# Optimization experiments

Measured on AMD Instinct MI355X. Metric: run time of the kernel, lower is better.

Reference implementation:

```python
import jax, jax.numpy as jnp
import numpy as np

B, N, D = 2, 2048, 1024
H = 16                      # num_heads, head_dim = 64
E, K, CF = 4, 2, 1.0        # num_experts, top_k, capacity_factor
MLP_H = int(D * 4.0)        # dense Mlp hidden (mlp_ratio=4.0)
MOE_H = int(D * 0.25)       # expert hidden (hard-coded dim*0.25 in source)


def setup_inputs() -> dict:
    key = jax.random.key(0)
    ks = jax.random.split(key, 12)
    r = lambda k, shp, s=0.02: jax.random.normal(k, shp, jnp.float32) * s
    return dict(
        x=jax.random.normal(ks[0], (B, N, D), jnp.float32),
        noise=jax.random.normal(ks[1], (B, N, E), jnp.float32),
        ln1_g=jnp.ones((D,), jnp.float32), ln1_b=jnp.zeros((D,), jnp.float32),
        ln2_g=jnp.ones((D,), jnp.float32), ln2_b=jnp.zeros((D,), jnp.float32),
        w_qkv=r(ks[2], (3 * D, D)),
        w_proj=r(ks[3], (D, D)), b_proj=jnp.zeros((D,), jnp.float32),
        w_route=r(ks[4], (D, E), 0.05), b_route=jnp.zeros((E,), jnp.float32),
        w_noise=r(ks[5], (D, E), 0.05), b_noise=jnp.zeros((E,), jnp.float32),
        we1=r(ks[6], (E, D, MOE_H)), be1=jnp.zeros((E, MOE_H), jnp.float32),
        we2=r(ks[7], (E, MOE_H, D)), be2=jnp.zeros((E, D), jnp.float32),
        w_mlp1=r(ks[8], (D, MLP_H)), b_mlp1=jnp.zeros((MLP_H,), jnp.float32),
        w_mlp2=r(ks[9], (MLP_H, D)), b_mlp2=jnp.zeros((D,), jnp.float32),
    )


def _ln(x, g, b, eps=1e-5):
    mu = x.mean(-1, keepdims=True)
    var = ((x - mu) ** 2).mean(-1, keepdims=True)
    return (x - mu) * jax.lax.rsqrt(var + eps) * g + b


def _gelu(x):
    return jax.nn.gelu(x, approximate=False)  # torch nn.GELU default (erf)


def reference(x, noise, ln1_g, ln1_b, ln2_g, ln2_b, w_qkv, w_proj, b_proj,
              w_route, b_route, w_noise, b_noise, we1, be1, we2, be2,
              w_mlp1, b_mlp1, w_mlp2, b_mlp2):
    Bs, Ns, Ds = x.shape
    hd = Ds // H
    # --- attention branch ---
    x1 = _ln(x, ln1_g, ln1_b)
    qkv = (x1 @ w_qkv.T).reshape(Bs, Ns, 3, H, hd).transpose(2, 0, 3, 1, 4)
    q, k, v = qkv[0] * (hd ** -0.5), qkv[1], qkv[2]
    attn = jax.nn.softmax(jnp.einsum('bhnd,bhmd->bhnm', q, k), axis=-1)
    ao = jnp.einsum('bhnm,bhmd->bhnd', attn, v).transpose(0, 2, 1, 3).reshape(Bs, Ns, Ds)
    x = x + (ao @ w_proj.T + b_proj)
    # --- shared norm for mlp + moe ---
    x2 = _ln(x, ln2_g, ln2_b)
    # --- noisy top-k router ---
    logits = x2 @ w_route + b_route                  # [B,N,E]
    noisy = logits + noise * jax.nn.softplus(x2 @ w_noise + b_noise)
    topv, topi = jax.lax.top_k(noisy, K)             # [B,N,K]
    probs = jax.nn.softmax(topv, axis=-1)            # softmax over sparse logits == softmax over top-k
    T = Bs * Ns
    flat_x = x2.reshape(T, Ds)
    fidx = topi.reshape(T, K)
    rows = jnp.arange(T)[:, None]
    gate = jnp.zeros((T, E), noisy.dtype).at[rows, fidx].set(probs.reshape(T, K))
    capacity = int(T * K / E * CF)
    # --- capacity-limited dispatch / expert MLP / combine ---
    def dispatch(eid, W1, b1, W2, b2):
        mask = jnp.any(fidx == eid, axis=-1)                     # [T]
        order = jnp.argsort(jnp.logical_not(mask))               # stable: selected tokens first, in token order
        sel = order[:capacity]                                   # [C]
        valid = mask[sel].astype(flat_x.dtype)
        h = _gelu(flat_x[sel] @ W1 + b1)
        out = h @ W2 + b2
        w = gate[sel, eid] * valid
        return sel, out * w[:, None]
    sel, outw = jax.vmap(dispatch)(jnp.arange(E), we1, be1, we2, be2)   # [E,C], [E,C,D]
    moe = jnp.zeros_like(flat_x).at[sel.reshape(-1)].add(outw.reshape(-1, Ds)).reshape(Bs, Ns, Ds)
    # --- dense mlp branch ---
    mlp = _gelu(x2 @ w_mlp1 + b_mlp1) @ w_mlp2 + b_mlp2
    return x + mlp + moe
```

## Files before the change

kernel.cpp:

```cpp
#include <hip/hip_runtime.h>
#include <hip/hip_bf16.h>
#include <math.h>

typedef __bf16 bf16;
typedef __bf16 bf16x4 __attribute__((ext_vector_type(4)));
typedef __bf16 bf16x8 __attribute__((ext_vector_type(8)));
typedef float  f32x4  __attribute__((ext_vector_type(4)));
typedef short  s16x4  __attribute__((ext_vector_type(4)));

#define T_TOK 4096
#define DIM   1024
#define NHEAD 16
#define SEQ   2048
#define NEXP  4
#define CAP   2048
#define MLPH  4096
#define MOEH  256

__device__ __forceinline__ float gelu_exact(float v) {
    return 0.5f * v * (1.f + erff(v * 0.70710678118654752f));
}

struct HL { bf16 h, l; };
__device__ __forceinline__ HL split2(float v) {
    HL r; r.h = (bf16)v; r.l = (bf16)(v - (float)r.h); return r;
}

__device__ __forceinline__ float fast_exp2(float x) {
#if __has_builtin(__builtin_amdgcn_exp2f)
    return __builtin_amdgcn_exp2f(x);
#else
    return exp2f(x);
#endif
}

__device__ __forceinline__ f32x4 mfma16(bf16x4 a, bf16x4 b, f32x4 c) {
    return __builtin_amdgcn_mfma_f32_16x16x16bf16_1k(
        __builtin_bit_cast(s16x4, a), __builtin_bit_cast(s16x4, b), c, 0, 0, 0);
}

__device__ __forceinline__ void gload16(const bf16* gptr, bf16* lptr) {
    __builtin_amdgcn_global_load_lds(
        (const __attribute__((address_space(1))) unsigned int*)gptr,
        (__attribute__((address_space(3))) unsigned int*)lptr,
        16, 0, 0);
}

__device__ __forceinline__ bf16x8 sw_frag(const bf16* arr, int row, int cc) {
    return *(const bf16x8*)&arr[row * 64 + ((cc ^ (row & 7)) * 8)];
}
__device__ __forceinline__ bf16x4 v_frag(const bf16* arr, int d, int q) {
    return *(const bf16x4*)&arr[d * 64 + ((q ^ (d & 15)) * 4)];
}

__global__ __launch_bounds__(256)
void ln_split_kernel(const float* __restrict__ x, const float* __restrict__ g,
                     const float* __restrict__ b, bf16* __restrict__ oh, bf16* __restrict__ ol) {
    int wave = threadIdx.x >> 6, lane = threadIdx.x & 63;
    long t = (long)blockIdx.x * 4 + wave;
    const float* xr = x + t * DIM;
    float v[16];
    #pragma unroll
    for (int i = 0; i < 16; i++) v[i] = xr[i * 64 + lane];
    float s = 0.f, s2 = 0.f;
    #pragma unroll
    for (int i = 0; i < 16; i++) { s += v[i]; s2 += v[i] * v[i]; }
    #pragma unroll
    for (int m = 1; m < 64; m <<= 1) { s += __shfl_xor(s, m); s2 += __shfl_xor(s2, m); }
    float mu  = s * (1.f / DIM);
    float var = s2 * (1.f / DIM) - mu * mu;
    float rs  = 1.f / sqrtf(var + 1e-5f);
    #pragma unroll
    for (int i = 0; i < 16; i++) {
        int d = i * 64 + lane;
        HL sp = split2((v[i] - mu) * rs * g[d] + b[d]);
        oh[t * DIM + d] = sp.h; ol[t * DIM + d] = sp.l;
    }
}

__global__ __launch_bounds__(256)
void split_pair_kernel(const float* __restrict__ in, bf16* __restrict__ h, bf16* __restrict__ l) {
    long i0 = ((long)blockIdx.x * 256 + threadIdx.x) * 4;
    f32x4 v = *(const f32x4*)&in[i0];
    bf16x4 vh, vl;
    #pragma unroll
    for (int j = 0; j < 4; j++) { HL sp = split2(v[j]); vh[j] = sp.h; vl[j] = sp.l; }
    *(bf16x4*)&h[i0] = vh; *(bf16x4*)&l[i0] = vl;
}

__global__ __launch_bounds__(256)
void transpose_conv_kernel(const float* __restrict__ in, bf16* __restrict__ out, int R, int C) {
    __shared__ bf16 tile[32][33];
    long bo = (long)blockIdx.z * R * C;
    in += bo; out += bo;
    int c0 = blockIdx.x * 32, r0 = blockIdx.y * 32;
    int tx = threadIdx.x & 31, ty = threadIdx.x >> 5;
    #pragma unroll
    for (int i = 0; i < 32; i += 8)
        tile[ty + i][tx] = (bf16)in[(long)(r0 + ty + i) * C + c0 + tx];
    __syncthreads();
    #pragma unroll
    for (int i = 0; i < 32; i += 8)
        out[(long)(c0 + ty + i) * R + r0 + tx] = tile[tx][ty + i];
}

__global__ __launch_bounds__(256)
void gemm_qkv(const bf16* __restrict__ Ah_g, const bf16* __restrict__ Al_g,
              const bf16* __restrict__ Bh_g, const bf16* __restrict__ Bl_g,
              bf16* __restrict__ Qh_g, bf16* __restrict__ Ql_g,
              bf16* __restrict__ Kh_g, bf16* __restrict__ Kl_g,
              bf16* __restrict__ VtH, bf16* __restrict__ VtL) {
    const int K = DIM;
    __shared__ alignas(16) bf16 Ah[8192], Al[8192], Bh[8192], Bl[8192];
    int tid = threadIdx.x;
    int wave = tid >> 6, lane = tid & 63;
    int l16 = lane & 15, l4 = lane >> 4;
    int wr = (wave >> 1) * 64, wc = (wave & 1) * 64;
    int row0 = blockIdx.y * 128, col0 = blockIdx.x * 128;
    int r8s = lane >> 3;
    int colb = ((lane & 7) ^ r8s) * 8;
    f32x4 acc[4][4] = {};
    for (int k0 = 0; k0 < K; k0 += 64) {
        #pragma unroll
        for (int p = 0; p < 4; p++) {
            int rl = p * 32 + wave * 8 + r8s;
            int lb = p * 2048 + wave * 512;
            gload16(&Ah_g[(long)(row0 + rl) * K + k0 + colb], &Ah[lb]);
            gload16(&Al_g[(long)(row0 + rl) * K + k0 + colb], &Al[lb]);
            gload16(&Bh_g[(long)(col0 + rl) * K + k0 + colb], &Bh[lb]);
            gload16(&Bl_g[(long)(col0 + rl) * K + k0 + colb], &Bl[lb]);
        }
        __syncthreads();
        #pragma unroll
        for (int ks = 0; ks < 2; ks++) {
            bf16x8 ah[4], al[4], bh[4], bl[4];
            #pragma unroll
            for (int i = 0; i < 4; i++) {
                ah[i] = sw_frag(Ah, wr + i*16 + l16, ks*4 + l4);
                al[i] = sw_frag(Al, wr + i*16 + l16, ks*4 + l4);
            }
            #pragma unroll
            for (int j = 0; j < 4; j++) {
                bh[j] = sw_frag(Bh, wc + j*16 + l16, ks*4 + l4);
                bl[j] = sw_frag(Bl, wc + j*16 + l16, ks*4 + l4);
            }
            #pragma unroll
            for (int i = 0; i < 4; i++)
                #pragma unroll
                for (int j = 0; j < 4; j++) {
                    acc[i][j] = __builtin_amdgcn_mfma_f32_16x16x32_bf16(ah[i], bh[j], acc[i][j], 0, 0, 0);
                    acc[i][j] = __builtin_amdgcn_mfma_f32_16x16x32_bf16(ah[i], bl[j], acc[i][j], 0, 0, 0);
                    acc[i][j] = __builtin_amdgcn_mfma_f32_16x16x32_bf16(al[i], bh[j], acc[i][j], 0, 0, 0);
                }
        }
        __syncthreads();
    }
    if (col0 < 2048) {
        bool isQ = (col0 < 1024);
        bf16* oh = isQ ? Qh_g : Kh_g;
        bf16* ol = isQ ? Ql_g : Kl_g;
        float qscale = isQ ? 0.18033688011112043f : 1.0f;
        #pragma unroll
        for (int i = 0; i < 4; i++)
            #pragma unroll
            for (int r = 0; r < 4; r++) {
                int t = row0 + wr + i * 16 + l4 * 4 + r;
                int bq = t >> 11, s = t & 2047;
                #pragma unroll
                for (int j = 0; j < 4; j++) {
                    int col = (col0 + wc + j * 16 + l16) & 1023;
                    int hh = col >> 6, dl = col & 63;
                    long o = ((long)(bq * NHEAD + hh) * SEQ + s) * 64 + dl;
                    HL sp = split2(acc[i][j][r] * qscale);
                    oh[o] = sp.h;
                    if (!isQ) ol[o] = sp.l;
                }
            }
    } else {
        #pragma unroll
        for (int i = 0; i < 4; i++) {
            int s0 = row0 + wr + i * 16 + l4 * 4;
            int b = s0 >> 11, sl = s0 & 2047;
            #pragma unroll
            for (int j = 0; j < 4; j++) {
                int d = col0 - 2048 + wc + j * 16 + l16;
                int h = d >> 6, dl = d & 63;
                long base = ((long)(b * NHEAD + h) * 64 + dl) * SEQ + (sl ^ ((dl & 1) << 2));
                bf16x4 vh, vl;
                #pragma unroll
                for (int r = 0; r < 4; r++) { HL sp = split2(acc[i][j][r]); vh[r] = sp.h; vl[r] = sp.l; }
                *(bf16x4*)&VtH[base] = vh;
                *(bf16x4*)&VtL[base] = vl;
            }
        }
    }
}

__global__ __launch_bounds__(512, 4)
void flash_attn(const bf16* __restrict__ Qh_g,
                const bf16* __restrict__ Kh_g, const bf16* __restrict__ Kl_g,
                const bf16* __restrict__ VtH_g, const bf16* __restrict__ VtL_g,
                bf16* __restrict__ aoh, bf16* __restrict__ aol) {
    __shared__ alignas(16) bf16 KhS[2][4096], KlS[2][4096], VhS[2][4096], VlS[2][4096];
    int tid = threadIdx.x;
    int wave = tid >> 6, lane = tid & 63;
    int l16 = lane & 15, l4 = lane >> 4;
    int bid = blockIdx.x;
    int bh = bid & 31;
    int b = bh >> 4, h = bh & 15;
    int q0 = (bid >> 5) * 128;

    bf16x8 qfh[2];
    {
        const bf16* qh = Qh_g + ((long)bh * SEQ + q0 + wave * 16 + l16) * 64;
        #pragma unroll
        for (int ks = 0; ks < 2; ks++)
            qfh[ks] = *(const bf16x8*)&qh[ks * 32 + l4 * 8];
    }
    int r8 = lane >> 3;
    int c8 = lane & 7;
    const bf16* kh_g = Kh_g + (long)bh * SEQ * 64;
    const bf16* kl_g = Kl_g + (long)bh * SEQ * 64;
    const bf16* vh_g = VtH_g + (long)bh * 64 * SEQ;
    const bf16* vl_g = VtL_g + (long)bh * 64 * SEQ;

    float m_s = -1e30f, l_s = 0.f;
    f32x4 accO[4] = {};

    auto stage = [&](int c0, int bsel) {
        int R0 = wave * 8;
        int row = R0 + r8;
        int ksw = (c8 ^ r8) * 8;
        int vsw = (c8 ^ ((wave * 4 + (r8 >> 1)) & 7)) * 8;
        gload16(&kh_g[(long)(c0 + row) * 64 + ksw], &KhS[bsel][R0 * 64]);
        gload16(&kl_g[(long)(c0 + row) * 64 + ksw], &KlS[bsel][R0 * 64]);
        gload16(&vh_g[(long)row * SEQ + c0 + vsw], &VhS[bsel][R0 * 64]);
        gload16(&vl_g[(long)row * SEQ + c0 + vsw], &VlS[bsel][R0 * 64]);
    };

    auto compute = [&](const bf16* KhT, const bf16* KlT, const bf16* VhT, const bf16* VlT) {
        f32x4 st[4] = {};
        __builtin_amdgcn_s_setprio(1);
        #pragma unroll
        for (int ks = 0; ks < 2; ks++) {
            #pragma unroll
            for (int i = 0; i < 4; i++) {
                bf16x8 akh = sw_frag(KhT, i * 16 + l16, ks * 4 + l4);
                bf16x8 akl = sw_frag(KlT, i * 16 + l16, ks * 4 + l4);
                st[i] = __builtin_amdgcn_mfma_f32_16x16x32_bf16(akh, qfh[ks], st[i], 0, 0, 0);
                st[i] = __builtin_amdgcn_mfma_f32_16x16x32_bf16(akl, qfh[ks], st[i], 0, 0, 0);
            }
        }
        __builtin_amdgcn_s_setprio(0);
        float mx = st[0][0];
        #pragma unroll
        for (int i = 0; i < 4; i++)
            #pragma unroll
            for (int r = 0; r < 4; r++) mx = fmaxf(mx, st[i][r]);
        mx = fmaxf(mx, __shfl_xor(mx, 16));
        mx = fmaxf(mx, __shfl_xor(mx, 32));
        if (!__all(mx <= m_s + 8.f)) {
            float mnew = fmaxf(m_s, mx);
            float alpha = fast_exp2(m_s - mnew);
            l_s *= alpha;
            #pragma unroll
            for (int i = 0; i < 4; i++)
                #pragma unroll
                for (int r = 0; r < 4; r++) accO[i][r] *= alpha;
            m_s = mnew;
        }
        float psum = 0.f;
        bf16x4 ph[4];
        #pragma unroll
        for (int kb = 0; kb < 4; kb++)
            #pragma unroll
            for (int r = 0; r < 4; r++) {
                float pv = fast_exp2(st[kb][r] - m_s);
                psum += pv;
                ph[kb][r] = (bf16)pv;
            }
        psum += __shfl_xor(psum, 16);
        psum += __shfl_xor(psum, 32);
        l_s += psum;
        __builtin_amdgcn_s_setprio(1);
        #pragma unroll
        for (int kb = 0; kb < 4; kb++) {
            #pragma unroll
            for (int i = 0; i < 4; i++) {
                bf16x4 avh = v_frag(VhT, i * 16 + l16, kb * 4 + l4);
                bf16x4 avl = v_frag(VlT, i * 16 + l16, kb * 4 + l4);
                accO[i] = mfma16(avh, ph[kb], accO[i]);
                accO[i] = mfma16(avl, ph[kb], accO[i]);
            }
        }
        __builtin_amdgcn_s_setprio(0);
    };

    const int NT = SEQ / 64;
    stage(0, 0);
    #pragma unroll 1
    for (int t = 0; t < NT; t += 2) {
        stage((t + 1) * 64, 1);
        asm volatile("s_waitcnt vmcnt(4)" ::: "memory");
        __builtin_amdgcn_sched_barrier(0);
        __builtin_amdgcn_s_barrier();
        compute(KhS[0], KlS[0], VhS[0], VlS[0]);
        asm volatile("" ::: "memory");
        __builtin_amdgcn_s_barrier();
        if (t + 2 < NT) {
            stage((t + 2) * 64, 0);
            asm volatile("s_waitcnt vmcnt(4)" ::: "memory");
        } else {
            asm volatile("s_waitcnt vmcnt(0)" ::: "memory");
        }
        __builtin_amdgcn_sched_barrier(0);
        __builtin_amdgcn_s_barrier();
        compute(KhS[1], KlS[1], VhS[1], VlS[1]);
        asm volatile("" ::: "memory");
        __builtin_amdgcn_s_barrier();
    }

    float inv = 1.f / l_s;
    int q = q0 + wave * 16 + l16;
    #pragma unroll
    for (int i = 0; i < 4; i++) {
        bf16x4 oh4, ol4;
        #pragma unroll
        for (int r = 0; r < 4; r++) { HL sp = split2(accO[i][r] * inv); oh4[r] = sp.h; ol4[r] = sp.l; }
        long o = ((long)(b * SEQ + q)) * DIM + h * 64 + i * 16 + l4 * 4;
        *(bf16x4*)&aoh[o] = oh4;
        *(bf16x4*)&aol[o] = ol4;
    }
}

__global__ __launch_bounds__(256)
void gemm_proj(const bf16* __restrict__ Ah_g, const bf16* __restrict__ Al_g,
               const bf16* __restrict__ Bh_g, const bf16* __restrict__ Bl_g,
               const float* __restrict__ bias, const float* __restrict__ res,
               float* __restrict__ C, int N, int K) {
    __shared__ alignas(16) bf16 Ah[8192], Al[8192], Bh[8192], Bl[8192];
    int tid = threadIdx.x;
    int wave = tid >> 6, lane = tid & 63;
    int l16 = lane & 15, l4 = lane >> 4;
    int wr = (wave >> 1) * 64, wc = (wave & 1) * 64;
    int row0 = blockIdx.y * 128, col0 = blockIdx.x * 128;
    int r8s = lane >> 3;
    int colb = ((lane & 7) ^ r8s) * 8;
    f32x4 acc[4][4] = {};
    for (int k0 = 0; k0 < K; k0 += 64) {
        #pragma unroll
        for (int p = 0; p < 4; p++) {
            int rl = p * 32 + wave * 8 + r8s;
            int lb = p * 2048 + wave * 512;
            gload16(&Ah_g[(long)(row0 + rl) * K + k0 + colb], &Ah[lb]);
            gload16(&Al_g[(long)(row0 + rl) * K + k0 + colb], &Al[lb]);
            gload16(&Bh_g[(long)(col0 + rl) * K + k0 + colb], &Bh[lb]);
            gload16(&Bl_g[(long)(col0 + rl) * K + k0 + colb], &Bl[lb]);
        }
        __syncthreads();
        #pragma unroll
        for (int ks = 0; ks < 2; ks++) {
            bf16x8 ah[4], al[4], bh[4], bl[4];
            #pragma unroll
            for (int i = 0; i < 4; i++) {
                ah[i] = sw_frag(Ah, wr + i*16 + l16, ks*4 + l4);
                al[i] = sw_frag(Al, wr + i*16 + l16, ks*4 + l4);
            }
            #pragma unroll
            for (int j = 0; j < 4; j++) {
                bh[j] = sw_frag(Bh, wc + j*16 + l16, ks*4 + l4);
                bl[j] = sw_frag(Bl, wc + j*16 + l16, ks*4 + l4);
            }
            #pragma unroll
            for (int i = 0; i < 4; i++)
                #pragma unroll
                for (int j = 0; j < 4; j++) {
                    acc[i][j] = __builtin_amdgcn_mfma_f32_16x16x32_bf16(ah[i], bh[j], acc[i][j], 0, 0, 0);
                    acc[i][j] = __builtin_amdgcn_mfma_f32_16x16x32_bf16(ah[i], bl[j], acc[i][j], 0, 0, 0);
                    acc[i][j] = __builtin_amdgcn_mfma_f32_16x16x32_bf16(al[i], bh[j], acc[i][j], 0, 0, 0);
                }
        }
        __syncthreads();
    }
    #pragma unroll
    for (int i = 0; i < 4; i++)
        #pragma unroll
        for (int r = 0; r < 4; r++) {
            int grow = row0 + wr + i * 16 + l4 * 4 + r;
            #pragma unroll
            for (int j = 0; j < 4; j++) {
                int gcol = col0 + wc + j * 16 + l16;
                long o = (long)grow * N + gcol;
                C[o] = acc[i][j][r] + bias[gcol] + res[o];
            }
        }
}

template<bool BIAS, bool GELU, bool GATHER, int OUT_MODE>
__global__ __launch_bounds__(256)
void gemm_bt(const bf16* __restrict__ A, const bf16* __restrict__ Bt,
             const float* __restrict__ bias,
             bf16* __restrict__ Cbf, float* __restrict__ Cf,
             const int* __restrict__ rowmap, const float* __restrict__ roww,
             int M, int N, int K,
             long eA, long eB, long ebias, long eMap, long eC) {
    int ez = blockIdx.z;
    A += (long)ez * eA; Bt += (long)ez * eB;
    if (BIAS) bias += (long)ez * ebias;
    if (GATHER || OUT_MODE == 3) rowmap += (long)ez * eMap;
    if (OUT_MODE == 3) roww += (long)ez * eMap;
    if (OUT_MODE == 0) Cbf += (long)ez * eC;

    __shared__ alignas(16) bf16 As[8192];
    __shared__ alignas(16) bf16 Bs[8192];
    int tid = threadIdx.x;
    int wave = tid >> 6, lane = tid & 63;
    int l16 = lane & 15, l4 = lane >> 4;
    int wr = (wave >> 1) * 64, wc = (wave & 1) * 64;
    int row0 = blockIdx.y * 128, col0 = blockIdx.x * 128;
    int r8s = lane >> 3;
    int colb = ((lane & 7) ^ r8s) * 8;

    long arow[4];
    #pragma unroll
    for (int p = 0; p < 4; p++) {
        long gr = row0 + p * 32 + wave * 8 + r8s;
        if (GATHER) gr = rowmap[gr];
        arow[p] = gr;
    }
    f32x4 acc[4][4] = {};
    for (int k0 = 0; k0 < K; k0 += 64) {
        #pragma unroll
        for (int p = 0; p < 4; p++) {
            int rl = p * 32 + wave * 8 + r8s;
            int lb = p * 2048 + wave * 512;
            gload16(&A[arow[p] * K + k0 + colb], &As[lb]);
            gload16(&Bt[(long)(col0 + rl) * K + k0 + colb], &Bs[lb]);
        }
        __syncthreads();
        #pragma unroll
        for (int ks = 0; ks < 2; ks++) {
            bf16x8 af[4], bfr[4];
            #pragma unroll
            for (int i = 0; i < 4; i++) af[i]  = sw_frag(As, wr + i*16 + l16, ks*4 + l4);
            #pragma unroll
            for (int j = 0; j < 4; j++) bfr[j] = sw_frag(Bs, wc + j*16 + l16, ks*4 + l4);
            #pragma unroll
            for (int i = 0; i < 4; i++)
                #pragma unroll
                for (int j = 0; j < 4; j++)
                    acc[i][j] = __builtin_amdgcn_mfma_f32_16x16x32_bf16(af[i], bfr[j], acc[i][j], 0, 0, 0);
        }
        __syncthreads();
    }
    #pragma unroll
    for (int i = 0; i < 4; i++)
        #pragma unroll
        for (int r = 0; r < 4; r++) {
            int grow = row0 + wr + i * 16 + l4 * 4 + r;
            int st = 0; float sw = 0.f;
            if (OUT_MODE == 3) { st = rowmap[grow]; sw = roww[grow]; }
            #pragma unroll
            for (int j = 0; j < 4; j++) {
                int gcol = col0 + wc + j * 16 + l16;
                float v = acc[i][j][r];
                if (BIAS) v += bias[gcol];
                if (GELU) v = gelu_exact(v);
                if (OUT_MODE == 0) {
                    Cbf[(long)grow * N + gcol] = (bf16)v;
                } else if (OUT_MODE == 2) {
                    long o = (long)grow * N + gcol;
                    Cf[o] += v;
                } else {
                    atomicAdd(&Cf[(long)st * N + gcol], sw * v);
                }
            }
        }
}

__global__ __launch_bounds__(256)
void routing_kernel(const float* __restrict__ xres, const float* __restrict__ g,
                    const float* __restrict__ b, const float* __restrict__ w_route,
                    const float* __restrict__ b_route, const float* __restrict__ w_noise,
                    const float* __restrict__ b_noise, const float* __restrict__ noise,
                    int* __restrict__ topi, float* __restrict__ topp,
                    bf16* __restrict__ x2b) {
    int wave = threadIdx.x >> 6, lane = threadIdx.x & 63;
    long t = (long)blockIdx.x * 4 + wave;
    const float* xr = xres + t * DIM;
    float v[16];
    #pragma unroll
    for (int i = 0; i < 16; i++) v[i] = xr[i * 64 + lane];
    float s = 0.f, s2 = 0.f;
    #pragma unroll
    for (int i = 0; i < 16; i++) { s += v[i]; s2 += v[i] * v[i]; }
    #pragma unroll
    for (int m = 1; m < 64; m <<= 1) { s += __shfl_xor(s, m); s2 += __shfl_xor(s2, m); }
    float mu  = s * (1.f / DIM);
    float var = s2 * (1.f / DIM) - mu * mu;
    float rs  = 1.f / sqrtf(var + 1e-5f);
    float accr[4] = {0.f,0.f,0.f,0.f}, accn[4] = {0.f,0.f,0.f,0.f};
    #pragma unroll
    for (int i = 0; i < 16; i++) {
        int d = i * 64 + lane;
        float n = (v[i] - mu) * rs * g[d] + b[d];
        x2b[t * DIM + d] = (bf16)n;
        #pragma unroll
        for (int e = 0; e < 4; e++) {
            accr[e] += n * w_route[d * 4 + e];
            accn[e] += n * w_noise[d * 4 + e];
        }
    }
    #pragma unroll
    for (int e = 0; e < 4; e++)
        #pragma unroll
        for (int m = 1; m < 64; m <<= 1) {
            accr[e] += __shfl_xor(accr[e], m);
            accn[e] += __shfl_xor(accn[e], m);
        }
    if (lane == 0) {
        float nz[4];
        #pragma unroll
        for (int e = 0; e < 4; e++) {
            float logit = accr[e] + b_route[e];
            float si = accn[e] + b_noise[e];
            float sp = si > 0.f ? si + log1pf(expf(-si)) : log1pf(expf(si));
            nz[e] = logit + noise[t * 4 + e] * sp;
        }
        int i1 = 0;
        #pragma unroll
        for (int e = 1; e < 4; e++) if (nz[e] > nz[i1]) i1 = e;
        int i2 = -1; float v2 = -1e30f;
        #pragma unroll
        for (int e = 0; e < 4; e++) if (e != i1 && nz[e] > v2) { v2 = nz[e]; i2 = e; }
        float ex = expf(v2 - nz[i1]);
        topi[t * 2]     = i1; topi[t * 2 + 1] = i2;
        topp[t * 2]     = 1.f / (1.f + ex);
        topp[t * 2 + 1] = ex / (1.f + ex);
    }
}

__global__ __launch_bounds__(256)
void dispatch_kernel(const int* __restrict__ topi, const float* __restrict__ topp,
                     int* __restrict__ sel, float* __restrict__ wgt) {
    int e = threadIdx.x >> 6, lane = threadIdx.x & 63;
    int cnt = 0;
    for (int c = 0; c < T_TOK; c += 64) {
        int t = c + lane;
        int i0 = topi[t * 2], i1 = topi[t * 2 + 1];
        bool m = (i0 == e) || (i1 == e);
        unsigned long long bal = __ballot(m);
        int pos = cnt + __popcll(bal & ((1ull << lane) - 1ull));
        if (m && pos < CAP) {
            sel[e * CAP + pos] = t;
            wgt[e * CAP + pos] = (i0 == e) ? topp[t * 2] : topp[t * 2 + 1];
        }
        cnt += (int)__popcll(bal);
    }
    if (cnt > CAP) cnt = CAP;
    for (int pos = cnt + lane; pos < CAP; pos += 64) {
        sel[e * CAP + pos] = 0;
        wgt[e * CAP + pos] = 0.f;
    }
}

extern "C" void kernel_launch(void* const* d_in, const int* in_sizes, int n_in,
                              void* d_out, int out_size, void* d_ws, size_t ws_size,
                              hipStream_t stream) {
    (void)in_sizes; (void)n_in; (void)out_size; (void)ws_size;
    const float* x       = (const float*)d_in[0];
    const float* noise   = (const float*)d_in[1];
    const float* ln1_g   = (const float*)d_in[2];
    const float* ln1_b   = (const float*)d_in[3];
    const float* ln2_g   = (const float*)d_in[4];
    const float* ln2_b   = (const float*)d_in[5];
    const float* w_qkv   = (const float*)d_in[6];
    const float* w_proj  = (const float*)d_in[7];
    const float* b_proj  = (const float*)d_in[8];
    const float* w_route = (const float*)d_in[9];
    const float* b_route = (const float*)d_in[10];
    const float* w_noise = (const float*)d_in[11];
    const float* b_noise = (const float*)d_in[12];
    const float* we1     = (const float*)d_in[13];
    const float* be1     = (const float*)d_in[14];
    const float* we2     = (const float*)d_in[15];
    const float* be2     = (const float*)d_in[16];
    const float* w_mlp1  = (const float*)d_in[17];
    const float* b_mlp1  = (const float*)d_in[18];
    const float* w_mlp2  = (const float*)d_in[19];
    const float* b_mlp2  = (const float*)d_in[20];
    float* d_outf = (float*)d_out;

    const size_t MB = 1024 * 1024;
    char* ws = (char*)d_ws;
    bf16* x1h = (bf16*)(ws);
    bf16* x1l = (bf16*)(ws + 8 * MB);
    bf16* aoh = (bf16*)(ws);
    bf16* aol = (bf16*)(ws + 8 * MB);
    bf16* w_mlp1T = (bf16*)(ws);
    bf16* w_mlp2T = (bf16*)(ws + 8 * MB);
    bf16* wqkvh = (bf16*)(ws + 16 * MB);
    bf16* wqkvl = (bf16*)(ws + 22 * MB);
    bf16* we1T  = (bf16*)(ws + 16 * MB);
    bf16* we2T  = (bf16*)(ws + 18 * MB);
    bf16* h_e   = (bf16*)(ws + 20 * MB);
    bf16* wprojh = (bf16*)(ws + 28 * MB);
    bf16* wprojl = (bf16*)(ws + 30 * MB);
    bf16* Qh = (bf16*)(ws + 32 * MB);
    bf16* Ql = (bf16*)(ws + 40 * MB);
    bf16* Kh = (bf16*)(ws + 48 * MB);
    bf16* Kl = (bf16*)(ws + 56 * MB);
    bf16* h_mlp = (bf16*)(ws + 32 * MB);
    bf16*  VtH  = (bf16*)(ws + 64 * MB);
    bf16*  VtL  = (bf16*)(ws + 72 * MB);
    bf16*  x2b  = (bf16*)(ws + 64 * MB);
    int*   topi = (int*)(ws + 72 * MB);
    float* topp = (float*)(ws + 72 * MB + 32768);
    int*   sel  = (int*)(ws + 72 * MB + 65536);
    float* wgt  = (float*)(ws + 72 * MB + 98304);

    ln_split_kernel<<<T_TOK/4, 256, 0, stream>>>(x, ln1_g, ln1_b, x1h, x1l);
    split_pair_kernel<<<(3*DIM*DIM)/1024, 256, 0, stream>>>(w_qkv, wqkvh, wqkvl);
    split_pair_kernel<<<(DIM*DIM)/1024,   256, 0, stream>>>(w_proj, wprojh, wprojl);

    gemm_qkv<<<dim3(3*DIM/128, T_TOK/128), 256, 0, stream>>>(
        x1h, x1l, wqkvh, wqkvl, Qh, Ql, Kh, Kl, VtH, VtL);

    flash_attn<<<dim3(32 * (SEQ/128)), 512, 0, stream>>>(Qh, Kh, Kl, VtH, VtL, aoh, aol);

    gemm_proj<<<dim3(DIM/128, T_TOK/128), 256, 0, stream>>>(
        aoh, aol, wprojh, wprojl, b_proj, x, d_outf, DIM, DIM);

    routing_kernel<<<T_TOK/4, 256, 0, stream>>>(d_outf, ln2_g, ln2_b, w_route, b_route,
                                                w_noise, b_noise, noise, topi, topp, x2b);
    dispatch_kernel<<<1, 256, 0, stream>>>(topi, topp, sel, wgt);

    transpose_conv_kernel<<<dim3(MLPH/32, DIM/32, 1),    256, 0, stream>>>(w_mlp1, w_mlp1T, DIM, MLPH);
    transpose_conv_kernel<<<dim3(DIM/32, MLPH/32, 1),    256, 0, stream>>>(w_mlp2, w_mlp2T, MLPH, DIM);
    transpose_conv_kernel<<<dim3(MOEH/32, DIM/32, NEXP), 256, 0, stream>>>(we1, we1T, DIM, MOEH);
    transpose_conv_kernel<<<dim3(DIM/32, MOEH/32, NEXP), 256, 0, stream>>>(we2, we2T, MOEH, DIM);

    gemm_bt<true,true,false,0><<<dim3(MLPH/128, T_TOK/128), 256, 0, stream>>>(
        x2b, w_mlp1T, b_mlp1, h_mlp, nullptr, nullptr, nullptr, T_TOK, MLPH, DIM,
        0, 0, 0, 0, 0);
    gemm_bt<true,false,false,2><<<dim3(DIM/128, T_TOK/128), 256, 0, stream>>>(
        h_mlp, w_mlp2T, b_mlp2, nullptr, d_outf, nullptr, nullptr, T_TOK, DIM, MLPH,
        0, 0, 0, 0, 0);

    gemm_bt<true,true,true,0><<<dim3(MOEH/128, CAP/128, NEXP), 256, 0, stream>>>(
        x2b, we1T, be1, h_e, nullptr, sel, nullptr, CAP, MOEH, DIM,
        0, (long)MOEH*DIM, MOEH, CAP, (long)CAP*MOEH);
    gemm_bt<true,false,false,3><<<dim3(DIM/128, CAP/128, NEXP), 256, 0, stream>>>(
        h_e, we2T, be2, nullptr, d_outf, sel, wgt, CAP, DIM, MOEH,
        (long)CAP*MOEH, (long)DIM*MOEH, DIM, CAP, 0);
}
```

Measured before the change: 635.2 us.

## Interleave V hi/lo splits and use 16x16x32 MFMA in PV product

The hi and lo bf16 halves of V are now stored interleaved in one transposed buffer. The attention kernel duplicates each P value to match that pairing, so a single 16x16x32 bf16 MFMA computes P·(Vh+Vl) where two 16x16x16 MFMAs were used before. This halves the PV MFMA issue count and fuses the two LDS fragment reads into one wider read. The cost is a new LDS swizzle and staging pattern, plus a V buffer of the same total size with a new layout.

```diff
diff --git a/kernel.cpp b/kernel.cpp
--- a/kernel.cpp
+++ b/kernel.cpp
@@ -6,7 +6,6 @@
 typedef __bf16 bf16x4 __attribute__((ext_vector_type(4)));
 typedef __bf16 bf16x8 __attribute__((ext_vector_type(8)));
 typedef float  f32x4  __attribute__((ext_vector_type(4)));
-typedef short  s16x4  __attribute__((ext_vector_type(4)));
 
 #define T_TOK 4096
 #define DIM   1024
@@ -34,11 +33,6 @@
 #endif
 }
 
-__device__ __forceinline__ f32x4 mfma16(bf16x4 a, bf16x4 b, f32x4 c) {
-    return __builtin_amdgcn_mfma_f32_16x16x16bf16_1k(
-        __builtin_bit_cast(s16x4, a), __builtin_bit_cast(s16x4, b), c, 0, 0, 0);
-}
-
 __device__ __forceinline__ void gload16(const bf16* gptr, bf16* lptr) {
     __builtin_amdgcn_global_load_lds(
         (const __attribute__((address_space(1))) unsigned int*)gptr,
@@ -48,9 +42,6 @@
 
 __device__ __forceinline__ bf16x8 sw_frag(const bf16* arr, int row, int cc) {
     return *(const bf16x8*)&arr[row * 64 + ((cc ^ (row & 7)) * 8)];
-}
-__device__ __forceinline__ bf16x4 v_frag(const bf16* arr, int d, int q) {
-    return *(const bf16x4*)&arr[d * 64 + ((q ^ (d & 15)) * 4)];
 }
 
 __global__ __launch_bounds__(256)
@@ -109,7 +100,7 @@
               const bf16* __restrict__ Bh_g, const bf16* __restrict__ Bl_g,
               bf16* __restrict__ Qh_g, bf16* __restrict__ Ql_g,
               bf16* __restrict__ Kh_g, bf16* __restrict__ Kl_g,
-              bf16* __restrict__ VtH, bf16* __restrict__ VtL) {
+              bf16* __restrict__ VtI) {
     const int K = DIM;
     __shared__ alignas(16) bf16 Ah[8192], Al[8192], Bh[8192], Bl[8192];
     int tid = threadIdx.x;
@@ -185,12 +176,14 @@
             for (int j = 0; j < 4; j++) {
                 int d = col0 - 2048 + wc + j * 16 + l16;
                 int h = d >> 6, dl = d & 63;
-                long base = ((long)(b * NHEAD + h) * 64 + dl) * SEQ + (sl ^ ((dl & 1) << 2));
-                bf16x4 vh, vl;
+                long base = ((long)(b * NHEAD + h) * 64 + dl) * (2 * SEQ) + 2 * sl;
+                bf16x8 vi;
                 #pragma unroll
-                for (int r = 0; r < 4; r++) { HL sp = split2(acc[i][j][r]); vh[r] = sp.h; vl[r] = sp.l; }
-                *(bf16x4*)&VtH[base] = vh;
-                *(bf16x4*)&VtL[base] = vl;
+                for (int r = 0; r < 4; r++) {
+                    HL sp = split2(acc[i][j][r]);
+                    vi[2 * r] = sp.h; vi[2 * r + 1] = sp.l;
+                }
+                *(bf16x8*)&VtI[base] = vi;
             }
         }
     }
@@ -199,9 +192,9 @@
 __global__ __launch_bounds__(512, 4)
 void flash_attn(const bf16* __restrict__ Qh_g,
                 const bf16* __restrict__ Kh_g, const bf16* __restrict__ Kl_g,
-                const bf16* __restrict__ VtH_g, const bf16* __restrict__ VtL_g,
+                const bf16* __restrict__ VtI_g,
                 bf16* __restrict__ aoh, bf16* __restrict__ aol) {
-    __shared__ alignas(16) bf16 KhS[2][4096], KlS[2][4096], VhS[2][4096], VlS[2][4096];
+    __shared__ alignas(16) bf16 KhS[2][4096], KlS[2][4096], VIS[2][8192];
     int tid = threadIdx.x;
     int wave = tid >> 6, lane = tid & 63;
     int l16 = lane & 15, l4 = lane >> 4;
@@ -219,10 +212,10 @@
     }
     int r8 = lane >> 3;
     int c8 = lane & 7;
+    int r4 = lane >> 4, c16 = lane & 15;
     const bf16* kh_g = Kh_g + (long)bh * SEQ * 64;
     const bf16* kl_g = Kl_g + (long)bh * SEQ * 64;
-    const bf16* vh_g = VtH_g + (long)bh * 64 * SEQ;
-    const bf16* vl_g = VtL_g + (long)bh * 64 * SEQ;
+    const bf16* vI_g = VtI_g + (long)bh * 64 * (2 * SEQ);
 
     float m_s = -1e30f, l_s = 0.f;
     f32x4 accO[4] = {};
@@ -231,14 +224,17 @@
         int R0 = wave * 8;
         int row = R0 + r8;
         int ksw = (c8 ^ r8) * 8;
-        int vsw = (c8 ^ ((wave * 4 + (r8 >> 1)) & 7)) * 8;
         gload16(&kh_g[(long)(c0 + row) * 64 + ksw], &KhS[bsel][R0 * 64]);
         gload16(&kl_g[(long)(c0 + row) * 64 + ksw], &KlS[bsel][R0 * 64]);
-        gload16(&vh_g[(long)row * SEQ + c0 + vsw], &VhS[bsel][R0 * 64]);
-        gload16(&vl_g[(long)row * SEQ + c0 + vsw], &VlS[bsel][R0 * 64]);
+        #pragma unroll
+        for (int q = 0; q < 2; q++) {
+            int d0 = R0 + q * 4 + r4;
+            gload16(&vI_g[(long)d0 * (2 * SEQ) + 2 * c0 + ((c16 ^ (d0 & 15)) * 8)],
+                    &VIS[bsel][(R0 + q * 4) * 128]);
+        }
     };
 
-    auto compute = [&](const bf16* KhT, const bf16* KlT, const bf16* VhT, const bf16* VlT) {
+    auto compute = [&](const bf16* KhT, const bf16* KlT, const bf16* VIT) {
         f32x4 st[4] = {};
         __builtin_amdgcn_s_setprio(1);
         #pragma unroll
@@ -270,14 +266,15 @@
             m_s = mnew;
         }
         float psum = 0.f;
-        bf16x4 ph[4];
+        bf16x8 pw[4];
         #pragma unroll
         for (int kb = 0; kb < 4; kb++)
             #pragma unroll
             for (int r = 0; r < 4; r++) {
                 float pv = fast_exp2(st[kb][r] - m_s);
                 psum += pv;
-                ph[kb][r] = (bf16)pv;
+                bf16 pb = (bf16)pv;
+                pw[kb][2 * r] = pb; pw[kb][2 * r + 1] = pb;
             }
         psum += __shfl_xor(psum, 16);
         psum += __shfl_xor(psum, 32);
@@ -287,10 +284,9 @@
         for (int kb = 0; kb < 4; kb++) {
             #pragma unroll
             for (int i = 0; i < 4; i++) {
-                bf16x4 avh = v_frag(VhT, i * 16 + l16, kb * 4 + l4);
-                bf16x4 avl = v_frag(VlT, i * 16 + l16, kb * 4 + l4);
-                accO[i] = mfma16(avh, ph[kb], accO[i]);
-                accO[i] = mfma16(avl, ph[kb], accO[i]);
+                int d = i * 16 + l16;
+                bf16x8 av = *(const bf16x8*)&VIT[d * 128 + (((kb * 4 + l4) ^ (d & 15)) * 8)];
+                accO[i] = __builtin_amdgcn_mfma_f32_16x16x32_bf16(av, pw[kb], accO[i], 0, 0, 0);
             }
         }
         __builtin_amdgcn_s_setprio(0);
@@ -304,7 +300,7 @@
         asm volatile("s_waitcnt vmcnt(4)" ::: "memory");
         __builtin_amdgcn_sched_barrier(0);
         __builtin_amdgcn_s_barrier();
-        compute(KhS[0], KlS[0], VhS[0], VlS[0]);
+        compute(KhS[0], KlS[0], VIS[0]);
         asm volatile("" ::: "memory");
         __builtin_amdgcn_s_barrier();
         if (t + 2 < NT) {
@@ -315,7 +311,7 @@
         }
         __builtin_amdgcn_sched_barrier(0);
         __builtin_amdgcn_s_barrier();
-        compute(KhS[1], KlS[1], VhS[1], VlS[1]);
+        compute(KhS[1], KlS[1], VIS[1]);
         asm volatile("" ::: "memory");
         __builtin_amdgcn_s_barrier();
     }
@@ -611,8 +607,7 @@
     bf16* Kh = (bf16*)(ws + 48 * MB);
     bf16* Kl = (bf16*)(ws + 56 * MB);
     bf16* h_mlp = (bf16*)(ws + 32 * MB);
-    bf16*  VtH  = (bf16*)(ws + 64 * MB);
-    bf16*  VtL  = (bf16*)(ws + 72 * MB);
+    bf16*  VtI  = (bf16*)(ws + 64 * MB);
     bf16*  x2b  = (bf16*)(ws + 64 * MB);
     int*   topi = (int*)(ws + 72 * MB);
     float* topp = (float*)(ws + 72 * MB + 32768);
@@ -624,9 +619,9 @@
     split_pair_kernel<<<(DIM*DIM)/1024,   256, 0, stream>>>(w_proj, wprojh, wprojl);
 
     gemm_qkv<<<dim3(3*DIM/128, T_TOK/128), 256, 0, stream>>>(
-        x1h, x1l, wqkvh, wqkvl, Qh, Ql, Kh, Kl, VtH, VtL);
-
-    flash_attn<<<dim3(32 * (SEQ/128)), 512, 0, stream>>>(Qh, Kh, Kl, VtH, VtL, aoh, aol);
+        x1h, x1l, wqkvh, wqkvl, Qh, Ql, Kh, Kl, VtI);
+
+    flash_attn<<<dim3(32 * (SEQ/128)), 512, 0, stream>>>(Qh, Kh, Kl, VtI, aoh, aol);
 
     gemm_proj<<<dim3(DIM/128, T_TOK/128), 256, 0, stream>>>(
         aoh, aol, wprojh, wprojl, b_proj, x, d_outf, DIM, DIM);
```

New measurement: 622.5 us. 2.0% less time.

## Drop bf16 low-part split for K and V in attention; add XCD tile swizzle

Applied to the files above, without the earlier changes.

Attention now stores K and V as single bf16 values instead of hi/lo pairs. This halves the K/V global loads, the LDS staging and the MFMA count in the QK and PV products of flash attention, and the wait counts are adjusted to match. The MoE/MLP gemm also remaps block indices so neighbouring tiles land on the same XCD, to improve L2 reuse. The cost is lower accuracy in the attention scores and outputs.

```diff
diff --git a/kernel.cpp b/kernel.cpp
--- a/kernel.cpp
+++ b/kernel.cpp
@@ -53,6 +53,16 @@
     return *(const bf16x4*)&arr[d * 64 + ((q ^ (d & 15)) * 4)];
 }
 
+__device__ __forceinline__ void xcd_tile(int& bx, int& by) {
+    int gx = gridDim.x;
+    int nwg = gx * gridDim.y;
+    int flat = blockIdx.y * gx + blockIdx.x;
+    int q = nwg >> 3, r = nwg & 7;
+    int xcd = flat & 7, loc = flat >> 3;
+    int swz = (xcd < r ? xcd * (q + 1) : r * (q + 1) + (xcd - r) * q) + loc;
+    bx = swz % gx; by = swz / gx;
+}
+
 __global__ __launch_bounds__(256)
 void ln_split_kernel(const float* __restrict__ x, const float* __restrict__ g,
                      const float* __restrict__ b, bf16* __restrict__ oh, bf16* __restrict__ ol) {
@@ -107,9 +117,8 @@
 __global__ __launch_bounds__(256)
 void gemm_qkv(const bf16* __restrict__ Ah_g, const bf16* __restrict__ Al_g,
               const bf16* __restrict__ Bh_g, const bf16* __restrict__ Bl_g,
-              bf16* __restrict__ Qh_g, bf16* __restrict__ Ql_g,
-              bf16* __restrict__ Kh_g, bf16* __restrict__ Kl_g,
-              bf16* __restrict__ VtH, bf16* __restrict__ VtL) {
+              bf16* __restrict__ Qh_g, bf16* __restrict__ Kh_g,
+              bf16* __restrict__ VtH) {
     const int K = DIM;
     __shared__ alignas(16) bf16 Ah[8192], Al[8192], Bh[8192], Bl[8192];
     int tid = threadIdx.x;
@@ -158,7 +167,6 @@
     if (col0 < 2048) {
         bool isQ = (col0 < 1024);
         bf16* oh = isQ ? Qh_g : Kh_g;
-        bf16* ol = isQ ? Ql_g : Kl_g;
         float qscale = isQ ? 0.18033688011112043f : 1.0f;
         #pragma unroll
         for (int i = 0; i < 4; i++)
@@ -171,9 +179,7 @@
                     int col = (col0 + wc + j * 16 + l16) & 1023;
                     int hh = col >> 6, dl = col & 63;
                     long o = ((long)(bq * NHEAD + hh) * SEQ + s) * 64 + dl;
-                    HL sp = split2(acc[i][j][r] * qscale);
-                    oh[o] = sp.h;
-                    if (!isQ) ol[o] = sp.l;
+                    oh[o] = (bf16)(acc[i][j][r] * qscale);
                 }
             }
     } else {
@@ -186,11 +192,10 @@
                 int d = col0 - 2048 + wc + j * 16 + l16;
                 int h = d >> 6, dl = d & 63;
                 long base = ((long)(b * NHEAD + h) * 64 + dl) * SEQ + (sl ^ ((dl & 1) << 2));
-                bf16x4 vh, vl;
+                bf16x4 vh;
                 #pragma unroll
-                for (int r = 0; r < 4; r++) { HL sp = split2(acc[i][j][r]); vh[r] = sp.h; vl[r] = sp.l; }
+                for (int r = 0; r < 4; r++) vh[r] = (bf16)acc[i][j][r];
                 *(bf16x4*)&VtH[base] = vh;
-                *(bf16x4*)&VtL[base] = vl;
             }
         }
     }
@@ -198,10 +203,10 @@
 
 __global__ __launch_bounds__(512, 4)
 void flash_attn(const bf16* __restrict__ Qh_g,
-                const bf16* __restrict__ Kh_g, const bf16* __restrict__ Kl_g,
-                const bf16* __restrict__ VtH_g, const bf16* __restrict__ VtL_g,
+                const bf16* __restrict__ Kh_g,
+                const bf16* __restrict__ VtH_g,
                 bf16* __restrict__ aoh, bf16* __restrict__ aol) {
-    __shared__ alignas(16) bf16 KhS[2][4096], KlS[2][4096], VhS[2][4096], VlS[2][4096];
+    __shared__ alignas(16) bf16 KhS[2][4096], VhS[2][4096];
     int tid = threadIdx.x;
     int wave = tid >> 6, lane = tid & 63;
     int l16 = lane & 15, l4 = lane >> 4;
@@ -220,9 +225,7 @@
     int r8 = lane >> 3;
     int c8 = lane & 7;
     const bf16* kh_g = Kh_g + (long)bh * SEQ * 64;
-    const bf16* kl_g = Kl_g + (long)bh * SEQ * 64;
     const bf16* vh_g = VtH_g + (long)bh * 64 * SEQ;
-    const bf16* vl_g = VtL_g + (long)bh * 64 * SEQ;
 
     float m_s = -1e30f, l_s = 0.f;
     f32x4 accO[4] = {};
@@ -233,12 +236,10 @@
         int ksw = (c8 ^ r8) * 8;
         int vsw = (c8 ^ ((wave * 4 + (r8 >> 1)) & 7)) * 8;
         gload16(&kh_g[(long)(c0 + row) * 64 + ksw], &KhS[bsel][R0 * 64]);
-        gload16(&kl_g[(long)(c0 + row) * 64 + ksw], &KlS[bsel][R0 * 64]);
         gload16(&vh_g[(long)row * SEQ + c0 + vsw], &VhS[bsel][R0 * 64]);
-        gload16(&vl_g[(long)row * SEQ + c0 + vsw], &VlS[bsel][R0 * 64]);
     };
 
-    auto compute = [&](const bf16* KhT, const bf16* KlT, const bf16* VhT, const bf16* VlT) {
+    auto compute = [&](const bf16* KhT, const bf16* VhT) {
         f32x4 st[4] = {};
         __builtin_amdgcn_s_setprio(1);
         #pragma unroll
@@ -246,9 +247,7 @@
             #pragma unroll
             for (int i = 0; i < 4; i++) {
                 bf16x8 akh = sw_frag(KhT, i * 16 + l16, ks * 4 + l4);
-                bf16x8 akl = sw_frag(KlT, i * 16 + l16, ks * 4 + l4);
                 st[i] = __builtin_amdgcn_mfma_f32_16x16x32_bf16(akh, qfh[ks], st[i], 0, 0, 0);
-                st[i] = __builtin_amdgcn_mfma_f32_16x16x32_bf16(akl, qfh[ks], st[i], 0, 0, 0);
             }
         }
         __builtin_amdgcn_s_setprio(0);
@@ -288,9 +287,7 @@
             #pragma unroll
             for (int i = 0; i < 4; i++) {
                 bf16x4 avh = v_frag(VhT, i * 16 + l16, kb * 4 + l4);
-                bf16x4 avl = v_frag(VlT, i * 16 + l16, kb * 4 + l4);
                 accO[i] = mfma16(avh, ph[kb], accO[i]);
-                accO[i] = mfma16(avl, ph[kb], accO[i]);
             }
         }
         __builtin_amdgcn_s_setprio(0);
@@ -301,21 +298,21 @@
     #pragma unroll 1
     for (int t = 0; t < NT; t += 2) {
         stage((t + 1) * 64, 1);
-        asm volatile("s_waitcnt vmcnt(4)" ::: "memory");
+        asm volatile("s_waitcnt vmcnt(2)" ::: "memory");
         __builtin_amdgcn_sched_barrier(0);
         __builtin_amdgcn_s_barrier();
-        compute(KhS[0], KlS[0], VhS[0], VlS[0]);
+        compute(KhS[0], VhS[0]);
         asm volatile("" ::: "memory");
         __builtin_amdgcn_s_barrier();
         if (t + 2 < NT) {
             stage((t + 2) * 64, 0);
-            asm volatile("s_waitcnt vmcnt(4)" ::: "memory");
+            asm volatile("s_waitcnt vmcnt(2)" ::: "memory");
         } else {
             asm volatile("s_waitcnt vmcnt(0)" ::: "memory");
         }
         __builtin_amdgcn_sched_barrier(0);
         __builtin_amdgcn_s_barrier();
-        compute(KhS[1], KlS[1], VhS[1], VlS[1]);
+        compute(KhS[1], VhS[1]);
         asm volatile("" ::: "memory");
         __builtin_amdgcn_s_barrier();
     }
@@ -417,7 +414,8 @@
     int wave = tid >> 6, lane = tid & 63;
     int l16 = lane & 15, l4 = lane >> 4;
     int wr = (wave >> 1) * 64, wc = (wave & 1) * 64;
-    int row0 = blockIdx.y * 128, col0 = blockIdx.x * 128;
+    int bx, by; xcd_tile(bx, by);
+    int row0 = by * 128, col0 = bx * 128;
     int r8s = lane >> 3;
     int colb = ((lane & 7) ^ r8s) * 8;
 
@@ -607,12 +605,9 @@
     bf16* wprojh = (bf16*)(ws + 28 * MB);
     bf16* wprojl = (bf16*)(ws + 30 * MB);
     bf16* Qh = (bf16*)(ws + 32 * MB);
-    bf16* Ql = (bf16*)(ws + 40 * MB);
-    bf16* Kh = (bf16*)(ws + 48 * MB);
-    bf16* Kl = (bf16*)(ws + 56 * MB);
+    bf16* Kh = (bf16*)(ws + 40 * MB);
     bf16* h_mlp = (bf16*)(ws + 32 * MB);
     bf16*  VtH  = (bf16*)(ws + 64 * MB);
-    bf16*  VtL  = (bf16*)(ws + 72 * MB);
     bf16*  x2b  = (bf16*)(ws + 64 * MB);
     int*   topi = (int*)(ws + 72 * MB);
     float* topp = (float*)(ws + 72 * MB + 32768);
@@ -624,9 +619,9 @@
     split_pair_kernel<<<(DIM*DIM)/1024,   256, 0, stream>>>(w_proj, wprojh, wprojl);
 
     gemm_qkv<<<dim3(3*DIM/128, T_TOK/128), 256, 0, stream>>>(
-        x1h, x1l, wqkvh, wqkvl, Qh, Ql, Kh, Kl, VtH, VtL);
-
-    flash_attn<<<dim3(32 * (SEQ/128)), 512, 0, stream>>>(Qh, Kh, Kl, VtH, VtL, aoh, aol);
+        x1h, x1l, wqkvh, wqkvl, Qh, Kh, VtH);
+
+    flash_attn<<<dim3(32 * (SEQ/128)), 512, 0, stream>>>(Qh, Kh, VtH, aoh, aol);
 
     gemm_proj<<<dim3(DIM/128, T_TOK/128), 256, 0, stream>>>(
         aoh, aol, wprojh, wprojl, b_proj, x, d_outf, DIM, DIM);
```

After: 593.2 us (median of 2 runs). 1.07x faster.
